# Kernel optimization log

Measured on AMD Instinct MI355X. Metric: run time of the kernel, lower is better.

## Reference

```python
import jax, jax.numpy as jnp
import numpy as np

NUM_CLASSES = 10


def setup_inputs() -> dict:
    key = jax.random.key(0)
    k1, k2, k3 = jax.random.split(key, 3)
    N, M, D = 1024, 50000, 512
    x = jax.random.normal(k1, (N, D), dtype=jnp.float32)
    exemplars = jax.random.normal(k2, (M, D), dtype=jnp.float32)
    labels = jax.random.randint(k3, (M,), 0, NUM_CLASSES)
    Sigma_inv = jnp.ones((D,), dtype=jnp.float32)
    beta = jnp.ones((1,), dtype=jnp.float32)
    gamma = jnp.ones((1,), dtype=jnp.float32)
    return {"x": x, "exemplars": exemplars, "labels": labels,
            "Sigma_inv": Sigma_inv, "beta": beta, "gamma": gamma}


def reference(x, exemplars, labels, Sigma_inv, beta, gamma):
    # Weighted squared Mahalanobis distance via expanded quadratic form:
    # dist[n,m] = sum_d Sigma_inv[d] * (x[n,d] - e[m,d])^2
    #           = (x^2 @ S) + (e^2 @ S) - 2 * (x*S) @ e^T
    x_sq = jnp.einsum('nd,d->n', x * x, Sigma_inv)            # [N]
    e_sq = jnp.einsum('md,d->m', exemplars * exemplars, Sigma_inv)  # [M]
    cross = jnp.einsum('nd,md->nm', x * Sigma_inv, exemplars)  # [N, M]
    distances = x_sq[:, None] + e_sq[None, :] - 2.0 * cross    # [N, M]
    attention = jnp.exp(-beta[0] * distances)                  # [N, M]
    # Per-class masked sum == segment sum over exemplar labels.
    logits = jax.ops.segment_sum(attention.T, labels,
                                 num_segments=NUM_CLASSES).T   # [N, 10]
    return jax.nn.softmax(gamma[0] * logits, axis=1)
```

## Files before the change

### kernel.cpp

```cpp
#include <hip/hip_runtime.h>
#include <hip/hip_bf16.h>
#include <stdint.h>
#include <stddef.h>

#define N_TOT 1024
#define M_TOT 50000
#define M_PAD 50176
#define MT_TILES 392
#define D_TOT 512
#define NC    10

typedef __attribute__((ext_vector_type(8))) __bf16 bf16x8;
typedef __attribute__((ext_vector_type(4))) float f32x4;
typedef __attribute__((ext_vector_type(4))) unsigned int u32x4;

union Frag16 { u32x4 q; bf16x8 b; unsigned short u[8]; };
union Pack8  { u32x4 q; unsigned short u[8]; };

__device__ __forceinline__ unsigned short f2bf(float x) {
  unsigned int u = __float_as_uint(x);
  unsigned int r = (u + 0x7fffu + ((u >> 16) & 1u)) >> 16;
  return (unsigned short)r;
}

__device__ __forceinline__ void gld_lds16(const void* g, void* l) {
  auto gp = (__attribute__((address_space(1))) unsigned int*)(uintptr_t)g;
  auto lp = (__attribute__((address_space(3))) unsigned int*)(uintptr_t)l;
  __builtin_amdgcn_global_load_lds(gp, lp, 16, 0, 0);
}

__global__ void prep_rows(const float* __restrict__ e, const float* __restrict__ x,
                          const float* __restrict__ S,
                          unsigned short* __restrict__ eb, unsigned short* __restrict__ xb,
                          float* __restrict__ e_sq, float* __restrict__ x_sq,
                          float* __restrict__ logits) {
  if (blockIdx.x < (N_TOT * NC + 255) / 256) {
    const int i = blockIdx.x * 256 + threadIdx.x;
    if (i < N_TOT * NC) logits[i] = 0.f;
  }

  const int lane = threadIdx.x & 63;
  const int wid  = threadIdx.x >> 6;
  const int row  = blockIdx.x * 4 + wid;
  const int d0   = lane * 8;

  float4 s0 = *(const float4*)(S + d0);
  float4 s1 = *(const float4*)(S + d0 + 4);
  float ss[8] = {s0.x, s0.y, s0.z, s0.w, s1.x, s1.y, s1.z, s1.w};

  float acc = 0.f;
  Pack8 o;

  if (row < M_PAD) {
    if (row < M_TOT) {
      const float* src = e + (size_t)row * D_TOT + d0;
      float4 v0 = *(const float4*)src;
      float4 v1 = *(const float4*)(src + 4);
      float vv[8] = {v0.x, v0.y, v0.z, v0.w, v1.x, v1.y, v1.z, v1.w};
      #pragma unroll
      for (int j = 0; j < 8; ++j) { acc += ss[j] * vv[j] * vv[j]; o.u[j] = f2bf(vv[j]); }
    } else {
      #pragma unroll
      for (int j = 0; j < 8; ++j) o.u[j] = 0;
      acc = 0.f;
    }
    *(u32x4*)(eb + (size_t)row * D_TOT + d0) = o.q;
    #pragma unroll
    for (int off = 32; off; off >>= 1) acc += __shfl_down(acc, off);
    if (lane == 0) e_sq[row] = (row < M_TOT) ? acc : 1e30f;
  } else {
    const int xr = row - M_PAD;
    const float* src = x + (size_t)xr * D_TOT + d0;
    float4 v0 = *(const float4*)src;
    float4 v1 = *(const float4*)(src + 4);
    float vv[8] = {v0.x, v0.y, v0.z, v0.w, v1.x, v1.y, v1.z, v1.w};
    #pragma unroll
    for (int j = 0; j < 8; ++j) {
      float w = ss[j] * vv[j];
      acc += w * vv[j];
      o.u[j] = f2bf(w);
    }
    *(u32x4*)(xb + (size_t)xr * D_TOT + d0) = o.q;
    #pragma unroll
    for (int off = 32; off; off >>= 1) acc += __shfl_down(acc, off);
    if (lane == 0) x_sq[xr] = acc;
  }
}

__launch_bounds__(256)
__global__ void gemm_fused(const unsigned short* __restrict__ xb,
                           const unsigned short* __restrict__ eb,
                           const float* __restrict__ x_sq, const float* __restrict__ e_sq,
                           const int* __restrict__ labels,
                           const float* __restrict__ betap,
                           float* __restrict__ logits) {
  __shared__ unsigned short As[3][128 * 32];
  __shared__ unsigned short Bs[3][128 * 32];
  __shared__ float cls[128 * NC];

  const int tid  = threadIdx.x;
  const int lane = tid & 63;
  const int wid  = tid >> 6;
  const int wr   = wid >> 1, wc = wid & 1;

  const int bid = blockIdx.x;
  const int c   = bid & 7;
  const int k_  = bid >> 3;
  const int mt  = c * 49 + (k_ >> 3);
  const int nt  = k_ & 7;

  const int cA0 = wid * 128 + lane;
  const int cA1 = cA0 + 64;
  const unsigned short* gA0 = xb + (size_t)(nt * 128 + (cA0 >> 2)) * D_TOT + (cA0 & 3) * 8;
  const unsigned short* gA1 = xb + (size_t)(nt * 128 + (cA1 >> 2)) * D_TOT + (cA1 & 3) * 8;
  const unsigned short* gB0 = eb + (size_t)(mt * 128 + (cA0 >> 2)) * D_TOT + (cA0 & 3) * 8;
  const unsigned short* gB1 = eb + (size_t)(mt * 128 + (cA1 >> 2)) * D_TOT + (cA1 & 3) * 8;

  const f32x4 vzero = {0.f, 0.f, 0.f, 0.f};
  f32x4 acc[4][4];
  #pragma unroll
  for (int i = 0; i < 4; ++i)
    #pragma unroll
    for (int j = 0; j < 4; ++j) acc[i][j] = vzero;

  const int arow = wr * 64 + (lane & 15);
  const int brow = wc * 64 + (lane & 15);
  const int koff = (lane >> 4) * 8;

  #define STAGE(BUF, K0)                                    \
    do {                                                    \
      gld_lds16(gA0 + (K0), &As[(BUF)][cA0 * 8]);           \
      gld_lds16(gA1 + (K0), &As[(BUF)][cA1 * 8]);           \
      gld_lds16(gB0 + (K0), &Bs[(BUF)][cA0 * 8]);           \
      gld_lds16(gB1 + (K0), &Bs[(BUF)][cA1 * 8]);           \
    } while (0)

  #define COMPUTE(BUF)                                                            \
    do {                                                                          \
      Frag16 fa[4], fb[4];                                                        \
      _Pragma("unroll")                                                           \
      for (int i = 0; i < 4; ++i)                                                 \
        fa[i].q = *(const u32x4*)(&As[(BUF)][(arow + i * 16) * 32 + koff]);       \
      _Pragma("unroll")                                                           \
      for (int j = 0; j < 4; ++j)                                                 \
        fb[j].q = *(const u32x4*)(&Bs[(BUF)][(brow + j * 16) * 32 + koff]);       \
      _Pragma("unroll")                                                           \
      for (int i = 0; i < 4; ++i)                                                 \
        _Pragma("unroll")                                                         \
        for (int j = 0; j < 4; ++j)                                               \
          acc[i][j] = __builtin_amdgcn_mfma_f32_16x16x32_bf16(fa[i].b, fb[j].b,   \
                                                              acc[i][j], 0, 0, 0);\
    } while (0)

  STAGE(0, 0);
  STAGE(1, 32);
  #pragma unroll
  for (int ks = 0; ks < 14; ++ks) {
    const int nb = (ks + 2) % 3;
    const int cb = ks % 3;
    STAGE(nb, (ks + 2) * 32);
    asm volatile("s_waitcnt vmcnt(8)" ::: "memory");
    __builtin_amdgcn_s_barrier();
    asm volatile("" ::: "memory");
    COMPUTE(cb);
    asm volatile("s_waitcnt lgkmcnt(0)" ::: "memory");
    __builtin_amdgcn_sched_barrier(0);
    __builtin_amdgcn_s_barrier();
  }
  asm volatile("s_waitcnt vmcnt(4)" ::: "memory");
  __builtin_amdgcn_s_barrier();
  asm volatile("" ::: "memory");
  COMPUTE(2);
  asm volatile("s_waitcnt vmcnt(0)" ::: "memory");
  __builtin_amdgcn_s_barrier();
  asm volatile("" ::: "memory");
  COMPUTE(0);
  #undef STAGE
  #undef COMPUTE

  __syncthreads();
  for (int t = tid; t < 128 * NC; t += 256) cls[t] = 0.f;
  __syncthreads();

  const float beta = betap[0];
  const int mbase = mt * 128 + wc * 64 + (lane & 15);
  int   lab[4]; float esq[4]; bool mv[4];
  #pragma unroll
  for (int j = 0; j < 4; ++j) {
    const int m = mbase + j * 16;
    mv[j]  = (m < M_TOT);
    esq[j] = e_sq[m];
    lab[j] = mv[j] ? labels[m] : 0;
  }

  #pragma unroll
  for (int i = 0; i < 4; ++i) {
    #pragma unroll
    for (int r = 0; r < 4; ++r) {
      const int nloc = wr * 64 + i * 16 + (lane >> 4) * 4 + r;
      const float xs = x_sq[nt * 128 + nloc];
      #pragma unroll
      for (int j = 0; j < 4; ++j) {
        if (!mv[j]) continue;
        const float dist = xs + esq[j] - 2.0f * acc[i][j][r];
        const float a = __expf(-beta * dist);
        if (a != 0.0f) atomicAdd(&cls[nloc * NC + lab[j]], a);
      }
    }
  }
  __syncthreads();
  for (int t = tid; t < 128 * NC; t += 256) {
    const float v = cls[t];
    if (v != 0.0f) atomicAdd(&logits[(size_t)(nt * 128 + (t / NC)) * NC + (t % NC)], v);
  }
}

__global__ void softmax_out(const float* __restrict__ logits,
                            const float* __restrict__ gammap,
                            float* __restrict__ out) {
  const int n = blockIdx.x * blockDim.x + threadIdx.x;
  if (n >= N_TOT) return;
  const float g = gammap[0];
  float v[NC], mx = -3.4e38f;
  #pragma unroll
  for (int c = 0; c < NC; ++c) { v[c] = g * logits[n * NC + c]; mx = fmaxf(mx, v[c]); }
  float s = 0.f;
  #pragma unroll
  for (int c = 0; c < NC; ++c) { v[c] = __expf(v[c] - mx); s += v[c]; }
  const float inv = 1.0f / s;
  #pragma unroll
  for (int c = 0; c < NC; ++c) out[n * NC + c] = v[c] * inv;
}

extern "C" void kernel_launch(void* const* d_in, const int* in_sizes, int n_in,
                              void* d_out, int out_size, void* d_ws, size_t ws_size,
                              hipStream_t stream) {
  const float* x      = (const float*)d_in[0];
  const float* e      = (const float*)d_in[1];
  const int*   labels = (const int*)d_in[2];
  const float* S      = (const float*)d_in[3];
  const float* beta   = (const float*)d_in[4];
  const float* gamma  = (const float*)d_in[5];

  char* ws = (char*)d_ws;
  unsigned short* eb     = (unsigned short*)(ws);
  unsigned short* xb     = (unsigned short*)(ws + 51380224);
  float*          e_sq   = (float*)(ws + 52428800);
  float*          x_sq   = (float*)(ws + 52629504);
  float*          logits = (float*)(ws + 52633600);

  hipLaunchKernelGGL(prep_rows, dim3((M_PAD + N_TOT) / 4), dim3(256), 0, stream,
                     e, x, S, eb, xb, e_sq, x_sq, logits);
  hipLaunchKernelGGL(gemm_fused, dim3(8 * MT_TILES), dim3(256), 0, stream,
                     xb, eb, x_sq, e_sq, labels, beta, logits);
  hipLaunchKernelGGL(softmax_out, dim3(4), dim3(256), 0, stream,
                     logits, gamma, (float*)d_out);
}
```

Before: 252.5 us.

## Enlarge GEMM block tile to 128x256 with 8 waves and double buffering

The fused distance GEMM now uses 512-thread blocks, each covering 128 query rows and 256 exemplar rows, which halves the number of exemplar tiles and the block count. The LDS pipeline goes from three stages to two, and the class-accumulation scratch now reuses the A-tile shared memory instead of its own array. The intent is to reuse each loaded x tile across more exemplars and to cut per-block epilogue and launch overhead. In exchange the prefetch depth is shallower, and the larger blocks may lower occupancy and lengthen the block tail.

```diff
diff --git a/kernel.cpp b/kernel.cpp
--- a/kernel.cpp
+++ b/kernel.cpp
@@ -6,7 +6,7 @@
 #define N_TOT 1024
 #define M_TOT 50000
 #define M_PAD 50176
-#define MT_TILES 392
+#define MT_TILES 196
 #define D_TOT 512
 #define NC    10
 
@@ -87,34 +87,34 @@
   }
 }
 
-__launch_bounds__(256)
+__launch_bounds__(512, 4)
 __global__ void gemm_fused(const unsigned short* __restrict__ xb,
                            const unsigned short* __restrict__ eb,
                            const float* __restrict__ x_sq, const float* __restrict__ e_sq,
                            const int* __restrict__ labels,
                            const float* __restrict__ betap,
                            float* __restrict__ logits) {
-  __shared__ unsigned short As[3][128 * 32];
-  __shared__ unsigned short Bs[3][128 * 32];
-  __shared__ float cls[128 * NC];
+  __shared__ unsigned short As[2][128 * 32];
+  __shared__ unsigned short Bs[2][256 * 32];
+  float* cls = (float*)&As[0][0];
 
   const int tid  = threadIdx.x;
   const int lane = tid & 63;
   const int wid  = tid >> 6;
-  const int wr   = wid >> 1, wc = wid & 1;
+  const int we   = wid >> 1;
+  const int wx   = wid & 1;
 
   const int bid = blockIdx.x;
-  const int c   = bid & 7;
-  const int k_  = bid >> 3;
-  const int mt  = c * 49 + (k_ >> 3);
-  const int nt  = k_ & 7;
-
-  const int cA0 = wid * 128 + lane;
-  const int cA1 = cA0 + 64;
-  const unsigned short* gA0 = xb + (size_t)(nt * 128 + (cA0 >> 2)) * D_TOT + (cA0 & 3) * 8;
-  const unsigned short* gA1 = xb + (size_t)(nt * 128 + (cA1 >> 2)) * D_TOT + (cA1 & 3) * 8;
-  const unsigned short* gB0 = eb + (size_t)(mt * 128 + (cA0 >> 2)) * D_TOT + (cA0 & 3) * 8;
-  const unsigned short* gB1 = eb + (size_t)(mt * 128 + (cA1 >> 2)) * D_TOT + (cA1 & 3) * 8;
+  const int g   = (bid & 7) * MT_TILES + (bid >> 3);
+  const int mt  = g >> 3;
+  const int nt  = g & 7;
+
+  const int cA  = wid * 64 + lane;
+  const int cB0 = wid * 128 + lane;
+  const int cB1 = cB0 + 64;
+  const unsigned short* gA  = xb + (size_t)(nt * 128 + (cA  >> 2)) * D_TOT + (cA  & 3) * 8;
+  const unsigned short* gB0 = eb + (size_t)(mt * 256 + (cB0 >> 2)) * D_TOT + (cB0 & 3) * 8;
+  const unsigned short* gB1 = eb + (size_t)(mt * 256 + (cB1 >> 2)) * D_TOT + (cB1 & 3) * 8;
 
   const f32x4 vzero = {0.f, 0.f, 0.f, 0.f};
   f32x4 acc[4][4];
@@ -123,16 +123,15 @@
     #pragma unroll
     for (int j = 0; j < 4; ++j) acc[i][j] = vzero;
 
-  const int arow = wr * 64 + (lane & 15);
-  const int brow = wc * 64 + (lane & 15);
+  const int arow = wx * 64 + (lane & 15);
+  const int brow = we * 64 + (lane & 15);
   const int koff = (lane >> 4) * 8;
 
   #define STAGE(BUF, K0)                                    \
     do {                                                    \
-      gld_lds16(gA0 + (K0), &As[(BUF)][cA0 * 8]);           \
-      gld_lds16(gA1 + (K0), &As[(BUF)][cA1 * 8]);           \
-      gld_lds16(gB0 + (K0), &Bs[(BUF)][cA0 * 8]);           \
-      gld_lds16(gB1 + (K0), &Bs[(BUF)][cA1 * 8]);           \
+      gld_lds16(gA  + (K0), &As[(BUF)][cA  * 8]);           \
+      gld_lds16(gB0 + (K0), &Bs[(BUF)][cB0 * 8]);           \
+      gld_lds16(gB1 + (K0), &Bs[(BUF)][cB1 * 8]);           \
     } while (0)
 
   #define COMPUTE(BUF)                                                            \
@@ -153,37 +152,30 @@
     } while (0)
 
   STAGE(0, 0);
-  STAGE(1, 32);
-  #pragma unroll
-  for (int ks = 0; ks < 14; ++ks) {
-    const int nb = (ks + 2) % 3;
-    const int cb = ks % 3;
-    STAGE(nb, (ks + 2) * 32);
-    asm volatile("s_waitcnt vmcnt(8)" ::: "memory");
+  #pragma unroll
+  for (int ks = 0; ks < 15; ++ks) {
+    STAGE((ks + 1) & 1, (ks + 1) * 32);
+    asm volatile("s_waitcnt vmcnt(3)" ::: "memory");
     __builtin_amdgcn_s_barrier();
     asm volatile("" ::: "memory");
-    COMPUTE(cb);
+    COMPUTE(ks & 1);
     asm volatile("s_waitcnt lgkmcnt(0)" ::: "memory");
     __builtin_amdgcn_sched_barrier(0);
     __builtin_amdgcn_s_barrier();
   }
-  asm volatile("s_waitcnt vmcnt(4)" ::: "memory");
-  __builtin_amdgcn_s_barrier();
-  asm volatile("" ::: "memory");
-  COMPUTE(2);
   asm volatile("s_waitcnt vmcnt(0)" ::: "memory");
   __builtin_amdgcn_s_barrier();
   asm volatile("" ::: "memory");
-  COMPUTE(0);
+  COMPUTE(1);
   #undef STAGE
   #undef COMPUTE
 
   __syncthreads();
-  for (int t = tid; t < 128 * NC; t += 256) cls[t] = 0.f;
+  for (int t = tid; t < 128 * NC; t += 512) cls[t] = 0.f;
   __syncthreads();
 
   const float beta = betap[0];
-  const int mbase = mt * 128 + wc * 64 + (lane & 15);
+  const int mbase = mt * 256 + we * 64 + (lane & 15);
   int   lab[4]; float esq[4]; bool mv[4];
   #pragma unroll
   for (int j = 0; j < 4; ++j) {
@@ -197,7 +189,7 @@
   for (int i = 0; i < 4; ++i) {
     #pragma unroll
     for (int r = 0; r < 4; ++r) {
-      const int nloc = wr * 64 + i * 16 + (lane >> 4) * 4 + r;
+      const int nloc = wx * 64 + i * 16 + (lane >> 4) * 4 + r;
       const float xs = x_sq[nt * 128 + nloc];
       #pragma unroll
       for (int j = 0; j < 4; ++j) {
@@ -209,7 +201,7 @@
     }
   }
   __syncthreads();
-  for (int t = tid; t < 128 * NC; t += 256) {
+  for (int t = tid; t < 128 * NC; t += 512) {
     const float v = cls[t];
     if (v != 0.0f) atomicAdd(&logits[(size_t)(nt * 128 + (t / NC)) * NC + (t % NC)], v);
   }
@@ -251,7 +243,7 @@
 
   hipLaunchKernelGGL(prep_rows, dim3((M_PAD + N_TOT) / 4), dim3(256), 0, stream,
                      e, x, S, eb, xb, e_sq, x_sq, logits);
-  hipLaunchKernelGGL(gemm_fused, dim3(8 * MT_TILES), dim3(256), 0, stream,
+  hipLaunchKernelGGL(gemm_fused, dim3(8 * MT_TILES), dim3(512), 0, stream,
                      xb, eb, x_sq, e_sq, labels, beta, logits);
   hipLaunchKernelGGL(softmax_out, dim3(4), dim3(256), 0, stream,
                      logits, gamma, (float*)d_out);
```

Result: faster. 233.5 us (-7.5%).
